# Kernel tuning notes

Hardware: AMD Instinct MI355X
Metric: run time of the kernel (lower is better)

## Reference

```python
import jax, jax.numpy as jnp
import numpy as np
from jax.scipy.special import logsumexp

S, D, K, R, P = 500, 768, 16, 256, 64  # seq_len, bert_dim, out_dim, n_pairs, max wordpieces/entity


def setup_inputs() -> dict:
    key = jax.random.key(0)
    k1, k2, k3, k4, k5, k6 = jax.random.split(key, 6)
    word_embeddings = jax.random.normal(k1, (S, D), jnp.float32)
    # kaiming_normal_ fan_in = D*K (last two dims collapsed); gain sqrt(2) for relu
    W = jax.random.normal(k2, (D, K, D), jnp.float32) * np.float32((2.0 / (K * D)) ** 0.5)
    idx1 = jax.random.randint(k3, (R, P), 0, S)
    idx2 = jax.random.randint(k4, (R, P), 0, S)
    # ragged mention lengths -> padding masks (at least 1 valid wordpiece)
    len1 = jax.random.randint(k5, (R,), 1, P + 1)
    len2 = jax.random.randint(k6, (R,), 1, P + 1)
    pos = jnp.arange(P)
    mask1 = (pos[None, :] < len1[:, None]).astype(jnp.float32)
    mask2 = (pos[None, :] < len2[:, None]).astype(jnp.float32)
    return {"word_embeddings": word_embeddings, "W": W, "idx1": idx1, "idx2": idx2,
            "mask1": mask1, "mask2": mask2}


def reference(word_embeddings, W, idx1, idx2, mask1, mask2):
    # gather ragged mention wordpieces (padded to P per entity)
    e1 = word_embeddings[idx1]  # [R, P, D]
    e2 = word_embeddings[idx2]  # [R, P, D]
    # biaffine: z[r,k,p,q] = e1[r,p,:] @ W[:,k,:] @ e2[r,q,:]
    zh = jnp.einsum('rpd,dke->rpke', e1, W)      # [R, P, K, D]
    z = jnp.einsum('rpke,rqe->rkpq', zh, e2)     # [R, K, P, P]
    # logsumexp pooling over all valid (p, q) mention-token pairs
    b = mask1[:, None, :, None] * mask2[:, None, None, :]  # [R, 1, P, P]
    scores = logsumexp(z, axis=(2, 3), b=b)      # [R, K]
    return scores
```

## Files before the change

kernel.cpp:

```cpp
#include <hip/hip_runtime.h>
#include <math.h>

#define S_ 500
#define D_ 768
#define K_ 16
#define R_ 256
#define P_ 64

typedef unsigned short ushort_t;
typedef __attribute__((ext_vector_type(8))) short short8;
typedef __attribute__((ext_vector_type(4))) float floatx4;

__device__ inline ushort_t f2bf(float x) {
  unsigned int u = __float_as_uint(x);
  u += 0x7fffu + ((u >> 16) & 1u);
  return (ushort_t)(u >> 16);
}

#define GLD_LDS16(g, l)                                                        \
  __builtin_amdgcn_global_load_lds(                                            \
      (const __attribute__((address_space(1))) void*)(g),                      \
      (__attribute__((address_space(3))) void*)(l), 16, 0, 0)

__global__ __launch_bounds__(256) void convert_we(const float* __restrict__ WE,
                                                  ushort_t* __restrict__ WEb) {
  int gid = blockIdx.x * 256 + threadIdx.x;
  int row = gid / 192;
  ushort4 o = {0, 0, 0, 0};
  if (row < S_) {
    float4 v = *(const float4*)(WE + (size_t)gid * 4);
    o.x = f2bf(v.x); o.y = f2bf(v.y); o.z = f2bf(v.z); o.w = f2bf(v.w);
  }
  *(ushort4*)(WEb + (size_t)gid * 4) = o;
}

__global__ __launch_bounds__(256) void transpose_w(const float* __restrict__ W,
                                                   ushort_t* __restrict__ Wt) {
  __shared__ float tile[32][33];
  const int t = threadIdx.x;
  const int n0 = blockIdx.x * 32, d0 = blockIdx.y * 32;
  const int r = t >> 3, c4 = (t & 7) * 4;
  float4 v = *(const float4*)(W + (size_t)(d0 + r) * 12288 + n0 + c4);
  tile[r][c4 + 0] = v.x; tile[r][c4 + 1] = v.y;
  tile[r][c4 + 2] = v.z; tile[r][c4 + 3] = v.w;
  __syncthreads();
  ushort4 o;
  o.x = f2bf(tile[c4 + 0][r]); o.y = f2bf(tile[c4 + 1][r]);
  o.z = f2bf(tile[c4 + 2][r]); o.w = f2bf(tile[c4 + 3][r]);
  *(ushort4*)(Wt + (size_t)(n0 + r) * 768 + d0 + c4) = o;
}

template <int MODE>
__global__ __launch_bounds__(256) void mm_bt(const ushort_t* __restrict__ A,
                                             const ushort_t* __restrict__ Bm,
                                             void* __restrict__ Cout) {
  __shared__ ushort_t As[128 * 32];
  __shared__ ushort_t Bs[128 * 32];
  const int tid = threadIdx.x;
  const int wave = tid >> 6, lane = tid & 63;
  const int m0 = blockIdx.y * 128, n0 = blockIdx.x * 128;
  const int wm = (wave & 1) * 64, wn = (wave >> 1) * 64;
  const int col = lane & 15, quad = lane >> 4;

  floatx4 acc[4][4];
#pragma unroll
  for (int i = 0; i < 4; i++)
#pragma unroll
    for (int j = 0; j < 4; j++)
#pragma unroll
      for (int e = 0; e < 4; e++) acc[i][j][e] = 0.f;

  const int srow = wave * 32 + (lane >> 2);
  const int scol = (lane & 3) * 8;

  for (int k0 = 0; k0 < D_; k0 += 32) {
    const ushort_t* ga = A + (size_t)(m0 + srow) * D_ + k0 + scol;
    const ushort_t* gb = Bm + (size_t)(n0 + srow) * D_ + k0 + scol;
    __syncthreads();
    GLD_LDS16(ga, &As[(wave * 32) * 32]);
    GLD_LDS16(ga + 16 * D_, &As[(wave * 32 + 16) * 32]);
    GLD_LDS16(gb, &Bs[(wave * 32) * 32]);
    GLD_LDS16(gb + 16 * D_, &Bs[(wave * 32 + 16) * 32]);
    __syncthreads();

    short8 a[4], b[4];
#pragma unroll
    for (int i = 0; i < 4; i++)
      a[i] = *(const short8*)&As[(wm + i * 16 + col) * 32 + quad * 8];
#pragma unroll
    for (int j = 0; j < 4; j++)
      b[j] = *(const short8*)&Bs[(wn + j * 16 + col) * 32 + quad * 8];
#pragma unroll
    for (int i = 0; i < 4; i++)
#pragma unroll
      for (int j = 0; j < 4; j++)
        acc[i][j] = __builtin_amdgcn_mfma_f32_16x16x32_bf16(a[i], b[j], acc[i][j], 0, 0, 0);
  }

  if (MODE == 0) {
    ushort_t* C = (ushort_t*)Cout;
#pragma unroll
    for (int i = 0; i < 4; i++) {
      int mb = m0 + wm + i * 16 + quad * 4;
#pragma unroll
      for (int j = 0; j < 4; j++) {
        int n = n0 + wn + j * 16 + col;
        C[(size_t)(mb + 0) * 12288 + n] = f2bf(acc[i][j][0]);
        C[(size_t)(mb + 1) * 12288 + n] = f2bf(acc[i][j][1]);
        C[(size_t)(mb + 2) * 12288 + n] = f2bf(acc[i][j][2]);
        C[(size_t)(mb + 3) * 12288 + n] = f2bf(acc[i][j][3]);
      }
    }
  } else {
    float* G = (float*)Cout;
#pragma unroll
    for (int i = 0; i < 4; i++) {
      int s1 = (m0 + wm + i * 16) >> 4;
#pragma unroll
      for (int j = 0; j < 4; j++) {
        int s2 = n0 + wn + j * 16 + col;
        if (s1 < S_ && s2 < S_)
          *(floatx4*)(G + (((size_t)s1 * S_ + s2) << 4) + quad * 4) = acc[i][j];
      }
    }
  }
}

__global__ __launch_bounds__(256) void lse_kernel(const float* __restrict__ G,
                                                  const int* __restrict__ idx1,
                                                  const int* __restrict__ idx2,
                                                  const float* __restrict__ mask1,
                                                  const float* __restrict__ mask2,
                                                  float* __restrict__ out) {
  const int r = blockIdx.x;
  const int tid = threadIdx.x;
  __shared__ int b1[P_], b2[P_];
  __shared__ int s_len1, s_len2;
  __shared__ float wm[4][K_], wsum[4][K_];

  if (tid < 64) {
    float mv = mask1[r * P_ + tid];
    unsigned long long bal = __ballot(mv > 0.5f);
    if (tid == 0) s_len1 = (int)__popcll(bal);
    b1[tid] = idx1[r * P_ + tid] * (S_ * K_);
  } else if (tid < 128) {
    int q = tid - 64;
    float mv = mask2[r * P_ + q];
    unsigned long long bal = __ballot(mv > 0.5f);
    if (q == 0) s_len2 = (int)__popcll(bal);
    b2[q] = idx2[r * P_ + q] * K_;
  }
  __syncthreads();
  const int len1 = s_len1, len2 = s_len2;
  const int total = len1 * len2;

  float m[K_], s[K_];
#pragma unroll
  for (int k = 0; k < K_; k++) { m[k] = -3.0e38f; s[k] = 0.f; }

  for (int i = tid; i < total; i += 256) {
    int p = i / len2;
    int q = i - p * len2;
    const float4* g4 = (const float4*)(G + b1[p] + b2[q]);
    float4 z0 = g4[0], z1 = g4[1], z2 = g4[2], z3 = g4[3];
    float z[K_] = {z0.x, z0.y, z0.z, z0.w, z1.x, z1.y, z1.z, z1.w,
                   z2.x, z2.y, z2.z, z2.w, z3.x, z3.y, z3.z, z3.w};
#pragma unroll
    for (int k = 0; k < K_; k++) {
      float zk = z[k];
      float M2 = fmaxf(m[k], zk);
      s[k] = s[k] * __expf(m[k] - M2) + __expf(zk - M2);
      m[k] = M2;
    }
  }

#pragma unroll
  for (int off = 1; off < 64; off <<= 1) {
#pragma unroll
    for (int k = 0; k < K_; k++) {
      float mo = __shfl_xor(m[k], off, 64);
      float so = __shfl_xor(s[k], off, 64);
      float M2 = fmaxf(m[k], mo);
      s[k] = s[k] * __expf(m[k] - M2) + so * __expf(mo - M2);
      m[k] = M2;
    }
  }
  const int wave = tid >> 6, lane = tid & 63;
  if (lane == 0) {
#pragma unroll
    for (int k = 0; k < K_; k++) { wm[wave][k] = m[k]; wsum[wave][k] = s[k]; }
  }
  __syncthreads();
  if (tid < K_) {
    float M = -3.0e38f, Ssum = 0.f;
#pragma unroll
    for (int w = 0; w < 4; w++) {
      float mo = wm[w][tid], so = wsum[w][tid];
      float M2 = fmaxf(M, mo);
      Ssum = Ssum * __expf(M - M2) + so * __expf(mo - M2);
      M = M2;
    }
    out[r * K_ + tid] = M + __logf(Ssum);
  }
}

extern "C" void kernel_launch(void* const* d_in, const int* in_sizes, int n_in,
                              void* d_out, int out_size, void* d_ws, size_t ws_size,
                              hipStream_t stream) {
  const float* WE    = (const float*)d_in[0];
  const float* W     = (const float*)d_in[1];
  const int*   idx1  = (const int*)d_in[2];
  const int*   idx2  = (const int*)d_in[3];
  const float* mask1 = (const float*)d_in[4];
  const float* mask2 = (const float*)d_in[5];
  float* out = (float*)d_out;

  ushort_t* WEb   = (ushort_t*)d_ws;
  ushort_t* Wt    = WEb + (size_t)512 * 768;
  ushort_t* projb = Wt + (size_t)12288 * 768;
  float*    G     = (float*)(projb + (size_t)8192 * 768);

  convert_we<<<384, 256, 0, stream>>>(WE, WEb);
  transpose_w<<<dim3(384, 24), 256, 0, stream>>>(W, Wt);
  mm_bt<0><<<dim3(96, 4), 256, 0, stream>>>(WEb, Wt, (void*)projb);
  mm_bt<1><<<dim3(4, 64), 256, 0, stream>>>(projb, WEb, (void*)G);
  lse_kernel<<<R_, 256, 0, stream>>>(G, idx1, idx2, mask1, mask2, out);
}
```

Before: 151.5 us.

## Merge prep kernels, widen transpose tiles, vectorize GEMM stores, split LSE across blocks

Fuses the embedding conversion and weight transpose into a single launch, and the transpose now uses 64x64 tiles with float4 shared-memory accesses. The first GEMM swaps its MFMA operands so each lane writes four consecutive bf16 outputs as one ushort4 store instead of four scattered stores. The log-sum-exp stage is split four ways per pair, with a small combine kernel added, so that more blocks run on the GPU. This trades an extra launch and partial-result buffers for better occupancy and wider memory traffic.

```diff
diff --git a/kernel.cpp b/kernel.cpp
--- a/kernel.cpp
+++ b/kernel.cpp
@@ -22,32 +22,51 @@
       (const __attribute__((address_space(1))) void*)(g),                      \
       (__attribute__((address_space(3))) void*)(l), 16, 0, 0)
 
-__global__ __launch_bounds__(256) void convert_we(const float* __restrict__ WE,
-                                                  ushort_t* __restrict__ WEb) {
-  int gid = blockIdx.x * 256 + threadIdx.x;
-  int row = gid / 192;
-  ushort4 o = {0, 0, 0, 0};
-  if (row < S_) {
-    float4 v = *(const float4*)(WE + (size_t)gid * 4);
-    o.x = f2bf(v.x); o.y = f2bf(v.y); o.z = f2bf(v.z); o.w = f2bf(v.w);
-  }
-  *(ushort4*)(WEb + (size_t)gid * 4) = o;
-}
-
-__global__ __launch_bounds__(256) void transpose_w(const float* __restrict__ W,
-                                                   ushort_t* __restrict__ Wt) {
-  __shared__ float tile[32][33];
+__global__ __launch_bounds__(256) void prep(const float* __restrict__ WE,
+                                            const float* __restrict__ W,
+                                            ushort_t* __restrict__ WEb,
+                                            ushort_t* __restrict__ Wt) {
   const int t = threadIdx.x;
-  const int n0 = blockIdx.x * 32, d0 = blockIdx.y * 32;
-  const int r = t >> 3, c4 = (t & 7) * 4;
-  float4 v = *(const float4*)(W + (size_t)(d0 + r) * 12288 + n0 + c4);
-  tile[r][c4 + 0] = v.x; tile[r][c4 + 1] = v.y;
-  tile[r][c4 + 2] = v.z; tile[r][c4 + 3] = v.w;
+  if (blockIdx.x < 384) {
+    int gid = blockIdx.x * 256 + t;
+    int row = gid / 192;
+    ushort4 o = {0, 0, 0, 0};
+    if (row < S_) {
+      float4 v = *(const float4*)(WE + (size_t)gid * 4);
+      o.x = f2bf(v.x); o.y = f2bf(v.y); o.z = f2bf(v.z); o.w = f2bf(v.w);
+    }
+    *(ushort4*)(WEb + (size_t)gid * 4) = o;
+    return;
+  }
+  __shared__ float tile[64][68];
+  const int tb = blockIdx.x - 384;
+  const int n0 = (tb % 192) * 64, d0 = (tb / 192) * 64;
+  {
+    const int r = t >> 2, cbase = (t & 3) * 16;
+#pragma unroll
+    for (int i = 0; i < 4; i++) {
+      float4 v = *(const float4*)(W + (size_t)(d0 + r) * 12288 + n0 + cbase + i * 4);
+      *(float4*)&tile[r][cbase + i * 4] = v;
+    }
+  }
   __syncthreads();
-  ushort4 o;
-  o.x = f2bf(tile[c4 + 0][r]); o.y = f2bf(tile[c4 + 1][r]);
-  o.z = f2bf(tile[c4 + 2][r]); o.w = f2bf(tile[c4 + 3][r]);
-  *(ushort4*)(Wt + (size_t)(n0 + r) * 768 + d0 + c4) = o;
+  {
+    const int bc = t & 15;
+    const int br4 = (t >> 4) * 4;
+    float4 tv[4];
+#pragma unroll
+    for (int ii = 0; ii < 4; ii++)
+      tv[ii] = *(const float4*)&tile[bc * 4 + ii][br4];
+#pragma unroll
+    for (int j = 0; j < 4; j++) {
+      ushort4 o;
+      o.x = f2bf(((const float*)&tv[0])[j]);
+      o.y = f2bf(((const float*)&tv[1])[j]);
+      o.z = f2bf(((const float*)&tv[2])[j]);
+      o.w = f2bf(((const float*)&tv[3])[j]);
+      *(ushort4*)(Wt + (size_t)(n0 + br4 + j) * 768 + d0 + bc * 4) = o;
+    }
+  }
 }
 
 template <int MODE>
@@ -93,22 +112,26 @@
 #pragma unroll
     for (int i = 0; i < 4; i++)
 #pragma unroll
-      for (int j = 0; j < 4; j++)
-        acc[i][j] = __builtin_amdgcn_mfma_f32_16x16x32_bf16(a[i], b[j], acc[i][j], 0, 0, 0);
+      for (int j = 0; j < 4; j++) {
+        if (MODE == 0)
+          acc[i][j] = __builtin_amdgcn_mfma_f32_16x16x32_bf16(b[j], a[i], acc[i][j], 0, 0, 0);
+        else
+          acc[i][j] = __builtin_amdgcn_mfma_f32_16x16x32_bf16(a[i], b[j], acc[i][j], 0, 0, 0);
+      }
   }
 
   if (MODE == 0) {
     ushort_t* C = (ushort_t*)Cout;
 #pragma unroll
     for (int i = 0; i < 4; i++) {
-      int mb = m0 + wm + i * 16 + quad * 4;
+      int m = m0 + wm + i * 16 + col;
 #pragma unroll
       for (int j = 0; j < 4; j++) {
-        int n = n0 + wn + j * 16 + col;
-        C[(size_t)(mb + 0) * 12288 + n] = f2bf(acc[i][j][0]);
-        C[(size_t)(mb + 1) * 12288 + n] = f2bf(acc[i][j][1]);
-        C[(size_t)(mb + 2) * 12288 + n] = f2bf(acc[i][j][2]);
-        C[(size_t)(mb + 3) * 12288 + n] = f2bf(acc[i][j][3]);
+        int n = n0 + wn + j * 16 + quad * 4;
+        ushort4 o;
+        o.x = f2bf(acc[i][j][0]); o.y = f2bf(acc[i][j][1]);
+        o.z = f2bf(acc[i][j][2]); o.w = f2bf(acc[i][j][3]);
+        *(ushort4*)(C + (size_t)m * 12288 + n) = o;
       }
     }
   } else {
@@ -126,17 +149,18 @@
   }
 }
 
-__global__ __launch_bounds__(256) void lse_kernel(const float* __restrict__ G,
-                                                  const int* __restrict__ idx1,
-                                                  const int* __restrict__ idx2,
-                                                  const float* __restrict__ mask1,
-                                                  const float* __restrict__ mask2,
-                                                  float* __restrict__ out) {
-  const int r = blockIdx.x;
+__global__ __launch_bounds__(256) void lse_part(const float* __restrict__ G,
+                                                const int* __restrict__ idx1,
+                                                const int* __restrict__ idx2,
+                                                const float* __restrict__ mask1,
+                                                const float* __restrict__ mask2,
+                                                float* __restrict__ pm,
+                                                float* __restrict__ ps) {
+  const int r = blockIdx.x >> 2, seg = blockIdx.x & 3;
   const int tid = threadIdx.x;
   __shared__ int b1[P_], b2[P_];
   __shared__ int s_len1, s_len2;
-  __shared__ float wm[4][K_], wsum[4][K_];
+  __shared__ float wmx[4][K_], wsum[4][K_];
 
   if (tid < 64) {
     float mv = mask1[r * P_ + tid];
@@ -151,14 +175,14 @@
     b2[q] = idx2[r * P_ + q] * K_;
   }
   __syncthreads();
-  const int len1 = s_len1, len2 = s_len2;
-  const int total = len1 * len2;
+  const int len2 = s_len2;
+  const int total = s_len1 * len2;
 
   float m[K_], s[K_];
 #pragma unroll
   for (int k = 0; k < K_; k++) { m[k] = -3.0e38f; s[k] = 0.f; }
 
-  for (int i = tid; i < total; i += 256) {
+  for (int i = seg * 256 + tid; i < total; i += 1024) {
     int p = i / len2;
     int q = i - p * len2;
     const float4* g4 = (const float4*)(G + b1[p] + b2[q]);
@@ -188,20 +212,38 @@
   const int wave = tid >> 6, lane = tid & 63;
   if (lane == 0) {
 #pragma unroll
-    for (int k = 0; k < K_; k++) { wm[wave][k] = m[k]; wsum[wave][k] = s[k]; }
+    for (int k = 0; k < K_; k++) { wmx[wave][k] = m[k]; wsum[wave][k] = s[k]; }
   }
   __syncthreads();
   if (tid < K_) {
     float M = -3.0e38f, Ssum = 0.f;
 #pragma unroll
     for (int w = 0; w < 4; w++) {
-      float mo = wm[w][tid], so = wsum[w][tid];
+      float mo = wmx[w][tid], so = wsum[w][tid];
       float M2 = fmaxf(M, mo);
       Ssum = Ssum * __expf(M - M2) + so * __expf(mo - M2);
       M = M2;
     }
-    out[r * K_ + tid] = M + __logf(Ssum);
-  }
+    pm[(r * 4 + seg) * K_ + tid] = M;
+    ps[(r * 4 + seg) * K_ + tid] = Ssum;
+  }
+}
+
+__global__ __launch_bounds__(256) void lse_combine(const float* __restrict__ pm,
+                                                   const float* __restrict__ ps,
+                                                   float* __restrict__ out) {
+  int gid = blockIdx.x * 256 + threadIdx.x;
+  int r = gid >> 4, k = gid & 15;
+  float M = -3.0e38f, Ssum = 0.f;
+#pragma unroll
+  for (int seg = 0; seg < 4; seg++) {
+    float mo = pm[(r * 4 + seg) * K_ + k];
+    float so = ps[(r * 4 + seg) * K_ + k];
+    float M2 = fmaxf(M, mo);
+    Ssum = Ssum * __expf(M - M2) + so * __expf(mo - M2);
+    M = M2;
+  }
+  out[gid] = M + __logf(Ssum);
 }
 
 extern "C" void kernel_launch(void* const* d_in, const int* in_sizes, int n_in,
@@ -219,10 +261,12 @@
   ushort_t* Wt    = WEb + (size_t)512 * 768;
   ushort_t* projb = Wt + (size_t)12288 * 768;
   float*    G     = (float*)(projb + (size_t)8192 * 768);
-
-  convert_we<<<384, 256, 0, stream>>>(WE, WEb);
-  transpose_w<<<dim3(384, 24), 256, 0, stream>>>(W, Wt);
+  float*    pm    = G + (size_t)S_ * S_ * K_;
+  float*    ps    = pm + R_ * 4 * K_;
+
+  prep<<<384 + 2304, 256, 0, stream>>>(WE, W, WEb, Wt);
   mm_bt<0><<<dim3(96, 4), 256, 0, stream>>>(WEb, Wt, (void*)projb);
   mm_bt<1><<<dim3(4, 64), 256, 0, stream>>>(projb, WEb, (void*)G);
-  lse_kernel<<<R_, 256, 0, stream>>>(G, idx1, idx2, mask1, mask2, out);
-}
+  lse_part<<<R_ * 4, 256, 0, stream>>>(G, idx1, idx2, mask1, mask2, pm, ps);
+  lse_combine<<<16, 256, 0, stream>>>(pm, ps, out);
+}
```

New measurement: 152.7 us. Within noise of the previous version (+0.8%).
